# Performance work log

Measured on AMD Instinct MI355X. Metric: run time of the kernel, lower is better.

## Reference

```python
import jax, jax.numpy as jnp
import numpy as np
from jax import lax

D_MODEL = 2048
D_STATE = 16
D_CONV = 4
B_SZ = 2
T_LEN = 2048


def setup_inputs() -> dict:
    key = jax.random.key(0)
    ks = jax.random.split(key, 8)
    x = jax.random.normal(ks[0], (B_SZ, T_LEN, D_MODEL), dtype=jnp.float32)
    h = jnp.zeros((B_SZ, D_MODEL, D_STATE), dtype=jnp.float32)
    norm_w = jnp.ones((D_MODEL,), dtype=jnp.float32)
    in_proj_w = jax.random.normal(ks[1], (2 * D_MODEL, D_MODEL), dtype=jnp.float32) * (D_MODEL ** -0.5)
    conv_w = jax.random.normal(ks[2], (D_MODEL, 1, D_CONV), dtype=jnp.float32) * 0.5
    conv_b = jnp.zeros((D_MODEL,), dtype=jnp.float32)
    x_proj_w = jax.random.normal(ks[3], (D_MODEL + 2 * D_STATE, D_MODEL), dtype=jnp.float32) * (D_MODEL ** -0.5)
    A_log = jnp.broadcast_to(jnp.log(jnp.arange(1, D_STATE + 1, dtype=jnp.float32))[None, :], (D_MODEL, D_STATE)).copy()
    D = jnp.ones((D_MODEL,), dtype=jnp.float32)
    out_proj_w = jax.random.normal(ks[4], (D_MODEL, D_MODEL), dtype=jnp.float32) * (D_MODEL ** -0.5)
    return {"x": x, "h": h, "norm_w": norm_w, "in_proj_w": in_proj_w,
            "conv_w": conv_w, "conv_b": conv_b, "x_proj_w": x_proj_w,
            "A_log": A_log, "D": D, "out_proj_w": out_proj_w}


def _rmsnorm(x, w, eps=1e-6):
    ms = jnp.mean(jnp.square(x.astype(jnp.float32)), axis=-1, keepdims=True)
    return (x * lax.rsqrt(ms + eps).astype(x.dtype)) * w.astype(x.dtype)


def reference(x, h, norm_w, in_proj_w, conv_w, conv_b, x_proj_w, A_log, D, out_proj_w):
    B, T, d_model = x.shape
    d_state = A_log.shape[1]
    residual = x
    x_normed = _rmsnorm(x, norm_w)
    xz = x_normed @ in_proj_w.T                      # (B, T, 2*d_model)
    x_branch, z = jnp.split(xz, 2, axis=-1)
    # depthwise causal conv1d: torch pads both sides by d_conv-1 then slices [:T],
    # equivalent to left-pad-only causal conv.
    xc = x_branch.transpose(0, 2, 1)                 # (B, d_model, T)
    xc = lax.conv_general_dilated(
        xc, conv_w, window_strides=(1,), padding=[(D_CONV - 1, 0)],
        dimension_numbers=("NCH", "OIH", "NCH"), feature_group_count=d_model)
    xc = xc + conv_b[None, :, None]
    x_ssm = jax.nn.silu(xc.transpose(0, 2, 1))       # (B, T, d_model)

    # SSM core
    proj = x_ssm @ x_proj_w.T                        # (B, T, d_model + 2*d_state)
    delta_raw = proj[..., :d_model]
    B_in = proj[..., d_model:d_model + d_state]
    C_in = proj[..., d_model + d_state:]
    delta = jax.nn.softplus(delta_raw)               # (B, T, d_model)
    A = -jnp.exp(A_log.astype(jnp.float32))          # (d_model, d_state)

    def step(h_c, inp):
        d_t, b_t, c_t, x_t = inp                     # (B,dm) (B,ds) (B,ds) (B,dm)
        A_bar = jnp.exp(d_t[:, :, None] * A[None])   # (B, dm, ds)
        h_c = A_bar * h_c + (d_t * x_t)[:, :, None] * b_t[:, None, :]
        y_t = jnp.einsum("bdn,bn->bd", h_c, c_t) + D * x_t
        return h_c, y_t

    xs = (delta.transpose(1, 0, 2), B_in.transpose(1, 0, 2),
          C_in.transpose(1, 0, 2), x_ssm.transpose(1, 0, 2))
    h_new, ys = lax.scan(step, h.astype(x.dtype), xs)
    y = ys.transpose(1, 0, 2)                        # (B, T, d_model)

    y = y * jax.nn.silu(z)
    out = residual + y @ out_proj_w.T
    return out, lax.stop_gradient(h_new)
```

## Files before the change

### kernel.cpp

```cpp
#include <hip/hip_runtime.h>
#include <cstdint>
#include <cstddef>


typedef __bf16 bf16_t;
typedef __attribute__((ext_vector_type(8))) __bf16 bf16x8;
typedef __attribute__((ext_vector_type(4))) __bf16 bf16x4;
typedef __attribute__((ext_vector_type(4))) float f32x4;

#define D_MODEL 2048
#define D_STATE 16
#define B_SZ 2
#define T_LEN 2048
#define N_ROWS (B_SZ * T_LEN)
#define N_PAD  2176
#define N_CHUNK 32
#define L_CHUNK (T_LEN / N_CHUNK)
#define LOG2E 1.4426950408889634f

__device__ __forceinline__ void load_lds16(const void* g, void* l) {
    __builtin_amdgcn_global_load_lds(
        (const __attribute__((address_space(1))) void*)(uintptr_t)g,
        (__attribute__((address_space(3))) void*)(uintptr_t)l,
        16, 0, 0);
}

__global__ __launch_bounds__(256) void cast_w13(
    const float* __restrict__ w1, const float* __restrict__ w3,
    bf16_t* __restrict__ d1, bf16_t* __restrict__ d3)
{
    int i = blockIdx.x * 256 + threadIdx.x;
    const int n1 = 4096 * 2048 / 4;
    if (i < n1) {
        f32x4 v = ((const f32x4*)w1)[i];
        ((bf16x4*)d1)[i] = __builtin_convertvector(v, bf16x4);
    } else {
        int j = i - n1;
        f32x4 v = ((const f32x4*)w3)[j];
        ((bf16x4*)d3)[j] = __builtin_convertvector(v, bf16x4);
    }
}

__global__ __launch_bounds__(256) void cast_pad_w2(
    const float* __restrict__ s, bf16_t* __restrict__ d)
{
    int i = blockIdx.x * 256 + threadIdx.x;
    int row = i >> 11;
    int col = i & 2047;
    float v = (row < 2080) ? s[(size_t)row * 2048 + col] : 0.f;
    d[i] = (bf16_t)v;
}

__global__ __launch_bounds__(256) void rmsnorm_kernel(
    const float* __restrict__ x, const float* __restrict__ w,
    bf16_t* __restrict__ xn)
{
    int row = blockIdx.x;
    int tid = threadIdx.x;
    const float* xr = x + (size_t)row * D_MODEL;
    float ss = 0.f;
    for (int i = tid; i < D_MODEL; i += 256) { float v = xr[i]; ss = fmaf(v, v, ss); }
    #pragma unroll
    for (int o = 32; o > 0; o >>= 1) ss += __shfl_down(ss, o, 64);
    __shared__ float red[4];
    if ((tid & 63) == 0) red[tid >> 6] = ss;
    __syncthreads();
    float tot = red[0] + red[1] + red[2] + red[3];
    float scale = rsqrtf(tot * (1.f / D_MODEL) + 1e-6f);
    bf16_t* xo = xn + (size_t)row * D_MODEL;
    for (int i = tid; i < D_MODEL; i += 256) xo[i] = (bf16_t)(xr[i] * scale * w[i]);
}

template<int MODE>
__global__ __launch_bounds__(256) void gemm_bt(
    const bf16_t* __restrict__ A, const bf16_t* __restrict__ B, int K,
    float* __restrict__ out0, bf16_t* __restrict__ out1,
    const float* __restrict__ add)
{
    __shared__ __align__(16) bf16_t lA[128 * 32];
    __shared__ __align__(16) bf16_t lB[128 * 32];
    __shared__ __align__(16) float cs[32 * 132];
    const int tid = threadIdx.x;
    const int bm = blockIdx.x, bn = blockIdx.y;

    const int rA = tid >> 2;
    const int cA = (tid & 3) * 8;
    const bf16_t* aSrc = A + ((size_t)bm * 128 + rA) * K + cA;
    const bf16_t* bSrc = B + ((size_t)bn * 128 + rA) * K + cA;

    const int lane = tid & 63;
    const int wave = tid >> 6;
    const int wm = (wave & 1) * 64;
    const int wn = (wave >> 1) * 64;
    const int fr = lane & 15;
    const int quad = lane >> 4;
    const int aOff = (wm + fr) * 32 + quad * 8;
    const int bOff = (wn + fr) * 32 + quad * 8;

    f32x4 acc[4][4];
    #pragma unroll
    for (int i = 0; i < 4; ++i)
        #pragma unroll
        for (int j = 0; j < 4; ++j) acc[i][j] = {0.f, 0.f, 0.f, 0.f};

    const int kIters = K >> 5;
    for (int kt = 0; kt < kIters; ++kt) {
        load_lds16(aSrc,                  &lA[tid * 8]);
        load_lds16(aSrc + (size_t)64 * K, &lA[2048 + tid * 8]);
        load_lds16(bSrc,                  &lB[tid * 8]);
        load_lds16(bSrc + (size_t)64 * K, &lB[2048 + tid * 8]);
        aSrc += 32; bSrc += 32;
        __syncthreads();

        bf16x8 af[4], bv[4];
        #pragma unroll
        for (int i = 0; i < 4; ++i) af[i] = *(const bf16x8*)(&lA[aOff + i * 512]);
        #pragma unroll
        for (int j = 0; j < 4; ++j) bv[j] = *(const bf16x8*)(&lB[bOff + j * 512]);
        #pragma unroll
        for (int i = 0; i < 4; ++i)
            #pragma unroll
            for (int j = 0; j < 4; ++j)
                acc[i][j] = __builtin_amdgcn_mfma_f32_16x16x32_bf16(
                    af[i], bv[j], acc[i][j], 0, 0, 0);
        __syncthreads();
    }

    const int lrow0 = (wave & 1) * 16 + quad * 4;
    const int lcol0 = wn + fr;
    for (int i = 0; i < 4; ++i) {
        __syncthreads();
        #pragma unroll
        for (int j = 0; j < 4; ++j)
            #pragma unroll
            for (int rr = 0; rr < 4; ++rr)
                cs[(lrow0 + rr) * 132 + lcol0 + j * 16] = acc[i][j][rr];
        __syncthreads();
        #pragma unroll
        for (int k = 0; k < 4; ++k) {
            int f4  = tid + k * 256;
            int row = f4 >> 5;
            int c4  = (f4 & 31) * 4;
            f32x4 v = *(const f32x4*)&cs[row * 132 + c4];
            int gr = bm * 128 + i * 16 + ((row < 16) ? row : (48 + row));
            int gc = bn * 128 + c4;
            if (MODE == 0) {
                if (bn < 16) {
                    *(f32x4*)&out0[(size_t)gr * 2048 + gc] = v;
                } else {
                    bf16x4 o;
                    #pragma unroll
                    for (int e = 0; e < 4; ++e) {
                        float s = v[e];
                        o[e] = (bf16_t)(s / (1.f + __expf(-s)));
                    }
                    *(bf16x4*)&out1[(size_t)gr * 2048 + (gc - 2048)] = o;
                }
            } else if (MODE == 1) {
                if (bn < 16) {
                    #pragma unroll
                    for (int e = 0; e < 4; ++e) {
                        float s = v[e];
                        v[e] = fmaxf(s, 0.f) + __logf(1.f + __expf(-fabsf(s)));
                    }
                }
                *(f32x4*)&out0[(size_t)gr * N_PAD + gc] = v;
            } else {
                f32x4 a4 = *(const f32x4*)&add[(size_t)gr * 2048 + gc];
                v = v + a4;
                *(f32x4*)&out0[(size_t)gr * 2048 + gc] = v;
            }
        }
    }
}

__global__ __launch_bounds__(256) void conv_silu_kernel(
    const float* __restrict__ xb, const float* __restrict__ cw,
    const float* __restrict__ cb, bf16_t* __restrict__ xs_b)
{
    int id = blockIdx.x * 256 + threadIdx.x;
    int d  = id & 2047;
    int tb = (id >> 11) & 255;
    int b  = id >> 19;
    float w0 = cw[d * 4 + 0], w1 = cw[d * 4 + 1], w2 = cw[d * 4 + 2], w3 = cw[d * 4 + 3];
    float bias = cb[d];
    int t0 = tb * 8;
    size_t base = (size_t)b * T_LEN;
    float v[11];
    #pragma unroll
    for (int i = 0; i < 11; ++i) {
        int t = t0 - 3 + i;
        v[i] = (t >= 0) ? xb[(base + t) * 2048 + d] : 0.f;
    }
    #pragma unroll
    for (int j = 0; j < 8; ++j) {
        float s = bias + w0 * v[j] + w1 * v[j + 1] + w2 * v[j + 2] + w3 * v[j + 3];
        float sl = s / (1.f + __expf(-s));
        xs_b[(base + t0 + j) * D_MODEL + d] = (bf16_t)sl;
    }
}

#define PF 4

__global__ __launch_bounds__(256) void scan_phase1(
    const float* __restrict__ proj, const bf16_t* __restrict__ xs,
    const float* __restrict__ A_log,
    float* __restrict__ Aprod, float* __restrict__ hfin)
{
    int wi   = blockIdx.x * 4 + (threadIdx.x >> 6);
    int lane = threadIdx.x & 63;
    int nq   = lane & 3;
    int dsub = lane >> 2;
    int c  = wi & 31;
    int dg = (wi >> 5) & 127;
    int b  = wi >> 12;
    int dd = dg * 16 + dsub;

    float A2[4], h[4], Ap[4];
    #pragma unroll
    for (int j = 0; j < 4; ++j) {
        A2[j] = -__expf(A_log[dd * D_STATE + nq * 4 + j]) * LOG2E;
        h[j] = 0.f; Ap[j] = 1.f;
    }
    const int t0 = c * L_CHUNK;
    const int tmax = t0 + L_CHUNK - 1;

    float p_da[PF], p_xv[PF];
    f32x4 p_B[PF];
    #pragma unroll
    for (int u = 0; u < PF; ++u) {
        size_t row = (size_t)b * T_LEN + t0 + u;
        const float* pr = proj + row * N_PAD;
        p_da[u] = pr[dd];
        p_xv[u] = (float)xs[row * D_MODEL + dd];
        p_B[u]  = *(const f32x4*)(pr + D_MODEL + nq * 4);
    }

    for (int it = 0; it < L_CHUNK; it += PF) {
        #pragma unroll
        for (int u = 0; u < PF; ++u) {
            int t = t0 + it + u;
            float da = p_da[u], xv = p_xv[u];
            f32x4 Bv = p_B[u];
            int tn = t + PF; tn = (tn > tmax) ? tmax : tn;
            {
                size_t row = (size_t)b * T_LEN + tn;
                const float* pr = proj + row * N_PAD;
                p_da[u] = pr[dd];
                p_xv[u] = (float)xs[row * D_MODEL + dd];
                p_B[u]  = *(const f32x4*)(pr + D_MODEL + nq * 4);
            }
            float dx = da * xv;
            #pragma unroll
            for (int j = 0; j < 4; ++j) {
                float a = exp2f(da * A2[j]);
                Ap[j] *= a;
                h[j] = fmaf(a, h[j], dx * Bv[j]);
            }
        }
    }
    size_t o = ((size_t)c * 4096 + b * 2048 + dd) * D_STATE + nq * 4;
    *(f32x4*)(Aprod + o) = f32x4{Ap[0], Ap[1], Ap[2], Ap[3]};
    *(f32x4*)(hfin  + o) = f32x4{h[0], h[1], h[2], h[3]};
}

__global__ __launch_bounds__(256) void scan_phase2(
    const float* __restrict__ h_in, const float* __restrict__ Aprod,
    float* __restrict__ hfin, float* __restrict__ h_out)
{
    int g = blockIdx.x * 256 + threadIdx.x;
    float h = h_in[g];
    for (int c = 0; c < N_CHUNK; ++c) {
        size_t o = (size_t)c * 65536 + g;
        float a   = Aprod[o];
        float loc = hfin[o];
        hfin[o] = h;
        h = fmaf(a, h, loc);
    }
    h_out[g] = h;
}

__global__ __launch_bounds__(256) void scan_phase3(
    const float* __restrict__ proj, const bf16_t* __restrict__ xs,
    const bf16_t* __restrict__ zg, const float* __restrict__ A_log,
    const float* __restrict__ Dv, const float* __restrict__ hinit,
    bf16_t* __restrict__ yg)
{
    int wi   = blockIdx.x * 4 + (threadIdx.x >> 6);
    int lane = threadIdx.x & 63;
    int nq   = lane & 3;
    int dsub = lane >> 2;
    int c  = wi & 31;
    int dg = (wi >> 5) & 127;
    int b  = wi >> 12;
    int dd = dg * 16 + dsub;

    float A2[4], h[4];
    size_t o = ((size_t)c * 4096 + b * 2048 + dd) * D_STATE + nq * 4;
    #pragma unroll
    for (int j = 0; j < 4; ++j) {
        A2[j] = -__expf(A_log[dd * D_STATE + nq * 4 + j]) * LOG2E;
        h[j]  = hinit[o + j];
    }
    float Dd = Dv[dd];
    const int t0 = c * L_CHUNK;
    const int tmax = t0 + L_CHUNK - 1;

    float p_da[PF], p_xv[PF], p_sz[PF];
    f32x4 p_B[PF], p_C[PF];
    #pragma unroll
    for (int u = 0; u < PF; ++u) {
        size_t row = (size_t)b * T_LEN + t0 + u;
        const float* pr = proj + row * N_PAD;
        p_da[u] = pr[dd];
        p_xv[u] = (float)xs[row * D_MODEL + dd];
        p_sz[u] = (float)zg[row * 2048 + dd];
        p_B[u]  = *(const f32x4*)(pr + D_MODEL + nq * 4);
        p_C[u]  = *(const f32x4*)(pr + D_MODEL + D_STATE + nq * 4);
    }

    for (int it = 0; it < L_CHUNK; it += PF) {
        #pragma unroll
        for (int u = 0; u < PF; ++u) {
            int t = t0 + it + u;
            float da = p_da[u], xv = p_xv[u], sz = p_sz[u];
            f32x4 Bv = p_B[u], Cv = p_C[u];
            int tn = t + PF; tn = (tn > tmax) ? tmax : tn;
            {
                size_t row = (size_t)b * T_LEN + tn;
                const float* pr = proj + row * N_PAD;
                p_da[u] = pr[dd];
                p_xv[u] = (float)xs[row * D_MODEL + dd];
                p_sz[u] = (float)zg[row * 2048 + dd];
                p_B[u]  = *(const f32x4*)(pr + D_MODEL + nq * 4);
                p_C[u]  = *(const f32x4*)(pr + D_MODEL + D_STATE + nq * 4);
            }
            float dx = da * xv;
            float yp = 0.f;
            #pragma unroll
            for (int j = 0; j < 4; ++j) {
                float a = exp2f(da * A2[j]);
                h[j] = fmaf(a, h[j], dx * Bv[j]);
                yp = fmaf(h[j], Cv[j], yp);
            }
            yp += __shfl_xor(yp, 1, 64);
            yp += __shfl_xor(yp, 2, 64);
            if (nq == 0) {
                float y = fmaf(Dd, xv, yp);
                yg[((size_t)b * T_LEN + t) * D_MODEL + dd] = (bf16_t)(y * sz);
            }
        }
    }
}

extern "C" void kernel_launch(void* const* d_in, const int* in_sizes, int n_in,
                              void* d_out, int out_size, void* d_ws, size_t ws_size,
                              hipStream_t stream)
{
    const float* x    = (const float*)d_in[0];
    const float* h0   = (const float*)d_in[1];
    const float* nw   = (const float*)d_in[2];
    const float* w_in = (const float*)d_in[3];
    const float* cw   = (const float*)d_in[4];
    const float* cb   = (const float*)d_in[5];
    const float* w_x  = (const float*)d_in[6];
    const float* alog = (const float*)d_in[7];
    const float* dv   = (const float*)d_in[8];
    const float* w_out= (const float*)d_in[9];
    float* out  = (float*)d_out;
    float* hout = out + (size_t)N_ROWS * D_MODEL;

    char* ws = (char*)d_ws;
    size_t off = 0;
    auto alloc = [&](size_t bytes) -> void* {
        void* p = ws + off;
        off += (bytes + 255) & ~(size_t)255;
        return p;
    };
    bf16_t* W1  = (bf16_t*)alloc((size_t)4096 * 2048 * 2);
    bf16_t* W2  = (bf16_t*)alloc((size_t)N_PAD * 2048 * 2);
    bf16_t* W3  = (bf16_t*)alloc((size_t)2048 * 2048 * 2);
    bf16_t* XN  = (bf16_t*)alloc((size_t)N_ROWS * 2048 * 2);
    float*  XB  = (float*) alloc((size_t)N_ROWS * 2048 * 4);
    bf16_t* ZG  = (bf16_t*)alloc((size_t)N_ROWS * 2048 * 2);
    float*  PROJ= (float*) alloc((size_t)N_ROWS * N_PAD * 4);
    float* APROD= (float*) alloc((size_t)N_CHUNK * 4096 * D_STATE * 4);
    float* HFIN = (float*) alloc((size_t)N_CHUNK * 4096 * D_STATE * 4);
    bf16_t* XSb = W1;
    bf16_t* YG  = XN;

    cast_w13<<<(4096 * 2048 / 4 + 2048 * 2048 / 4) / 256, 256, 0, stream>>>(w_in, w_out, W1, W3);
    cast_pad_w2<<<(N_PAD * 2048) / 256, 256, 0, stream>>>(w_x, W2);

    rmsnorm_kernel<<<N_ROWS, 256, 0, stream>>>(x, nw, XN);
    gemm_bt<0><<<dim3(32, 32), 256, 0, stream>>>(XN, W1, 2048, XB, ZG, nullptr);
    conv_silu_kernel<<<(B_SZ * (T_LEN / 8) * D_MODEL) / 256, 256, 0, stream>>>(XB, cw, cb, XSb);
    gemm_bt<1><<<dim3(32, N_PAD / 128), 256, 0, stream>>>(XSb, W2, 2048, PROJ, nullptr, nullptr);
    scan_phase1<<<2048, 256, 0, stream>>>(PROJ, XSb, alog, APROD, HFIN);
    scan_phase2<<<256, 256, 0, stream>>>(h0, APROD, HFIN, hout);
    scan_phase3<<<2048, 256, 0, stream>>>(PROJ, XSb, ZG, alog, dv, HFIN, YG);
    gemm_bt<2><<<dim3(32, 16), 256, 0, stream>>>(YG, W3, 2048, out, nullptr, x);

    (void)in_sizes; (void)n_in; (void)out_size; (void)ws_size;
}
```

Measured before the change: 515.8 us.

## Rewrite bf16 GEMM with 256x256 tiles and 4-stage LDS pipeline; vectorize rmsnorm

The MFMA GEMM moves to 512-thread blocks that compute 256x256 output tiles. It uses a 4-deep ring of global_load_lds stages with explicit vmcnt waits, so there is one barrier per k-step instead of two. It adds a swizzled LDS layout to avoid bank conflicts, raises wave priority around the MFMA burst, and uses a wider epilogue staging buffer. N_PAD grows to 2304 so the x_proj GEMM fits the larger tiles, which costs some extra padded work. The 128 KB LDS footprint allows only one block per CU, and the out_proj grid shrinks to 128 blocks, which leaves many CUs idle. The rmsnorm kernel now keeps each row in float4 registers and writes bf16x4 vectors.

```diff
diff --git a/kernel.cpp b/kernel.cpp
--- a/kernel.cpp
+++ b/kernel.cpp
@@ -13,7 +13,7 @@
 #define B_SZ 2
 #define T_LEN 2048
 #define N_ROWS (B_SZ * T_LEN)
-#define N_PAD  2176
+#define N_PAD  2304
 #define N_CHUNK 32
 #define L_CHUNK (T_LEN / N_CHUNK)
 #define LOG2E 1.4426950408889634f
@@ -24,6 +24,9 @@
         (__attribute__((address_space(3))) void*)(uintptr_t)l,
         16, 0, 0);
 }
+
+#define VMW(n) asm volatile("s_waitcnt vmcnt(" #n ")" ::: "memory")
+#define BAR()  do { __builtin_amdgcn_s_barrier(); __builtin_amdgcn_sched_barrier(0); } while (0)
 
 __global__ __launch_bounds__(256) void cast_w13(
     const float* __restrict__ w1, const float* __restrict__ w3,
@@ -57,9 +60,12 @@
 {
     int row = blockIdx.x;
     int tid = threadIdx.x;
-    const float* xr = x + (size_t)row * D_MODEL;
+    const f32x4* xr = (const f32x4*)(x + (size_t)row * D_MODEL);
+    f32x4 v0 = xr[tid];
+    f32x4 v1 = xr[tid + 256];
     float ss = 0.f;
-    for (int i = tid; i < D_MODEL; i += 256) { float v = xr[i]; ss = fmaf(v, v, ss); }
+    #pragma unroll
+    for (int e = 0; e < 4; ++e) { ss = fmaf(v0[e], v0[e], ss); ss = fmaf(v1[e], v1[e], ss); }
     #pragma unroll
     for (int o = 32; o > 0; o >>= 1) ss += __shfl_down(ss, o, 64);
     __shared__ float red[4];
@@ -67,110 +73,139 @@
     __syncthreads();
     float tot = red[0] + red[1] + red[2] + red[3];
     float scale = rsqrtf(tot * (1.f / D_MODEL) + 1e-6f);
-    bf16_t* xo = xn + (size_t)row * D_MODEL;
-    for (int i = tid; i < D_MODEL; i += 256) xo[i] = (bf16_t)(xr[i] * scale * w[i]);
+    const f32x4* w4 = (const f32x4*)w;
+    f32x4 m0 = v0 * w4[tid] * scale;
+    f32x4 m1 = v1 * w4[tid + 256] * scale;
+    bf16x4* xo = (bf16x4*)(xn + (size_t)row * D_MODEL);
+    xo[tid]       = __builtin_convertvector(m0, bf16x4);
+    xo[tid + 256] = __builtin_convertvector(m1, bf16x4);
 }
 
 template<int MODE>
-__global__ __launch_bounds__(256) void gemm_bt(
-    const bf16_t* __restrict__ A, const bf16_t* __restrict__ B, int K,
+__global__ __launch_bounds__(512, 2) void gemm_bt(
+    const bf16_t* __restrict__ A, const bf16_t* __restrict__ Bw, int K,
     float* __restrict__ out0, bf16_t* __restrict__ out1,
     const float* __restrict__ add)
 {
-    __shared__ __align__(16) bf16_t lA[128 * 32];
-    __shared__ __align__(16) bf16_t lB[128 * 32];
-    __shared__ __align__(16) float cs[32 * 132];
-    const int tid = threadIdx.x;
-    const int bm = blockIdx.x, bn = blockIdx.y;
-
-    const int rA = tid >> 2;
-    const int cA = (tid & 3) * 8;
-    const bf16_t* aSrc = A + ((size_t)bm * 128 + rA) * K + cA;
-    const bf16_t* bSrc = B + ((size_t)bn * 128 + rA) * K + cA;
-
+    __shared__ __align__(16) char smem[131072];
+    char* const ldsA = smem;
+    char* const ldsB = smem + 65536;
+
+    const int tid  = threadIdx.x;
+    const int bm   = blockIdx.x, bn = blockIdx.y;
     const int lane = tid & 63;
     const int wave = tid >> 6;
-    const int wm = (wave & 1) * 64;
-    const int wn = (wave >> 1) * 64;
-    const int fr = lane & 15;
+    const int wm   = wave >> 2;
+    const int wn   = wave & 3;
+    const int fr   = lane & 15;
     const int quad = lane >> 4;
-    const int aOff = (wm + fr) * 32 + quad * 8;
-    const int bOff = (wn + fr) * 32 + quad * 8;
-
-    f32x4 acc[4][4];
-    #pragma unroll
-    for (int i = 0; i < 4; ++i)
+
+    const int rS   = tid >> 2;
+    const int cS   = tid & 3;
+    const int gcol = ((cS - ((rS >> 1) & 3)) & 3) * 8;
+    const bf16_t* sA0 = A  + (size_t)(bm * 256 + rS) * K + gcol;
+    const bf16_t* sA1 = sA0 + (size_t)128 * K;
+    const bf16_t* sB0 = Bw + (size_t)(bn * 256 + rS) * K + gcol;
+    const bf16_t* sB1 = sB0 + (size_t)128 * K;
+
+    const int swz  = ((quad + ((fr >> 1) & 3)) & 3) * 8;
+    const int aOff = (wm * 128 + fr) * 32 + swz;
+    const int bOff = (wn * 64  + fr) * 32 + swz;
+
+    f32x4 acc[8][4];
+    #pragma unroll
+    for (int i = 0; i < 8; ++i)
         #pragma unroll
         for (int j = 0; j < 4; ++j) acc[i][j] = {0.f, 0.f, 0.f, 0.f};
 
-    const int kIters = K >> 5;
-    for (int kt = 0; kt < kIters; ++kt) {
-        load_lds16(aSrc,                  &lA[tid * 8]);
-        load_lds16(aSrc + (size_t)64 * K, &lA[2048 + tid * 8]);
-        load_lds16(bSrc,                  &lB[tid * 8]);
-        load_lds16(bSrc + (size_t)64 * K, &lB[2048 + tid * 8]);
-        aSrc += 32; bSrc += 32;
-        __syncthreads();
-
-        bf16x8 af[4], bv[4];
-        #pragma unroll
-        for (int i = 0; i < 4; ++i) af[i] = *(const bf16x8*)(&lA[aOff + i * 512]);
-        #pragma unroll
-        for (int j = 0; j < 4; ++j) bv[j] = *(const bf16x8*)(&lB[bOff + j * 512]);
-        #pragma unroll
-        for (int i = 0; i < 4; ++i)
+#define STAGE(b) do { \
+        load_lds16(sA0, ldsA + (b) * 16384 + tid * 16);        \
+        load_lds16(sA1, ldsA + (b) * 16384 + tid * 16 + 8192); \
+        load_lds16(sB0, ldsB + (b) * 16384 + tid * 16);        \
+        load_lds16(sB1, ldsB + (b) * 16384 + tid * 16 + 8192); \
+        sA0 += 32; sA1 += 32; sB0 += 32; sB1 += 32; } while (0)
+
+    auto compute = [&](int cb) {
+        const bf16_t* pA = (const bf16_t*)(ldsA + cb * 16384);
+        const bf16_t* pB = (const bf16_t*)(ldsB + cb * 16384);
+        bf16x8 bfr[4];
+        #pragma unroll
+        for (int j = 0; j < 4; ++j)
+            bfr[j] = *(const bf16x8*)(pB + bOff + j * 512);
+        __builtin_amdgcn_s_setprio(1);
+        #pragma unroll
+        for (int i = 0; i < 8; ++i) {
+            bf16x8 a = *(const bf16x8*)(pA + aOff + i * 512);
             #pragma unroll
             for (int j = 0; j < 4; ++j)
                 acc[i][j] = __builtin_amdgcn_mfma_f32_16x16x32_bf16(
-                    af[i], bv[j], acc[i][j], 0, 0, 0);
+                    a, bfr[j], acc[i][j], 0, 0, 0);
+        }
+        __builtin_amdgcn_s_setprio(0);
+    };
+
+    const int nt = K >> 5;
+    STAGE(0); STAGE(1); STAGE(2);
+    for (int t = 0; t < nt - 3; ++t) {
+        VMW(8); BAR();
+        STAGE((t + 3) & 3);
+        compute(t & 3);
+    }
+    VMW(8); BAR(); compute((nt - 3) & 3);
+    VMW(4); BAR(); compute((nt - 2) & 3);
+    VMW(0); BAR(); compute((nt - 1) & 3);
+#undef STAGE
+
+    float* const cs = (float*)smem;
+    __syncthreads();
+    for (int s = 0; s < 4; ++s) {
+        if (wm == (s >> 1)) {
+            const int i0 = (s & 1) * 4;
+            #pragma unroll
+            for (int ii = 0; ii < 4; ++ii)
+                #pragma unroll
+                for (int j = 0; j < 4; ++j)
+                    #pragma unroll
+                    for (int rr = 0; rr < 4; ++rr)
+                        cs[(ii * 16 + quad * 4 + rr) * 268 + wn * 64 + j * 16 + fr]
+                            = acc[i0 + ii][j][rr];
+        }
         __syncthreads();
-    }
-
-    const int lrow0 = (wave & 1) * 16 + quad * 4;
-    const int lcol0 = wn + fr;
-    for (int i = 0; i < 4; ++i) {
-        __syncthreads();
-        #pragma unroll
-        for (int j = 0; j < 4; ++j)
-            #pragma unroll
-            for (int rr = 0; rr < 4; ++rr)
-                cs[(lrow0 + rr) * 132 + lcol0 + j * 16] = acc[i][j][rr];
-        __syncthreads();
-        #pragma unroll
-        for (int k = 0; k < 4; ++k) {
-            int f4  = tid + k * 256;
-            int row = f4 >> 5;
-            int c4  = (f4 & 31) * 4;
-            f32x4 v = *(const f32x4*)&cs[row * 132 + c4];
-            int gr = bm * 128 + i * 16 + ((row < 16) ? row : (48 + row));
-            int gc = bn * 128 + c4;
+        #pragma unroll
+        for (int k = 0; k < 8; ++k) {
+            const int idx = tid + k * 512;
+            const int row = idx >> 6;
+            const int c4  = (idx & 63) << 2;
+            f32x4 v = *(const f32x4*)(cs + row * 268 + c4);
+            const int gr = bm * 256 + s * 64 + row;
+            const int gc = bn * 256 + c4;
             if (MODE == 0) {
-                if (bn < 16) {
+                if (bn < 8) {
                     *(f32x4*)&out0[(size_t)gr * 2048 + gc] = v;
                 } else {
                     bf16x4 o;
                     #pragma unroll
                     for (int e = 0; e < 4; ++e) {
-                        float s = v[e];
-                        o[e] = (bf16_t)(s / (1.f + __expf(-s)));
+                        float sv = v[e];
+                        o[e] = (bf16_t)(sv / (1.f + __expf(-sv)));
                     }
                     *(bf16x4*)&out1[(size_t)gr * 2048 + (gc - 2048)] = o;
                 }
             } else if (MODE == 1) {
-                if (bn < 16) {
+                if (bn < 8) {
                     #pragma unroll
                     for (int e = 0; e < 4; ++e) {
-                        float s = v[e];
-                        v[e] = fmaxf(s, 0.f) + __logf(1.f + __expf(-fabsf(s)));
+                        float sv = v[e];
+                        v[e] = fmaxf(sv, 0.f) + __logf(1.f + __expf(-fabsf(sv)));
                     }
                 }
                 *(f32x4*)&out0[(size_t)gr * N_PAD + gc] = v;
             } else {
                 f32x4 a4 = *(const f32x4*)&add[(size_t)gr * 2048 + gc];
-                v = v + a4;
-                *(f32x4*)&out0[(size_t)gr * 2048 + gc] = v;
+                *(f32x4*)&out0[(size_t)gr * 2048 + gc] = v + a4;
             }
         }
+        __syncthreads();
     }
 }
 
@@ -393,13 +428,13 @@
     cast_pad_w2<<<(N_PAD * 2048) / 256, 256, 0, stream>>>(w_x, W2);
 
     rmsnorm_kernel<<<N_ROWS, 256, 0, stream>>>(x, nw, XN);
-    gemm_bt<0><<<dim3(32, 32), 256, 0, stream>>>(XN, W1, 2048, XB, ZG, nullptr);
+    gemm_bt<0><<<dim3(16, 16), 512, 0, stream>>>(XN, W1, 2048, XB, ZG, nullptr);
     conv_silu_kernel<<<(B_SZ * (T_LEN / 8) * D_MODEL) / 256, 256, 0, stream>>>(XB, cw, cb, XSb);
-    gemm_bt<1><<<dim3(32, N_PAD / 128), 256, 0, stream>>>(XSb, W2, 2048, PROJ, nullptr, nullptr);
+    gemm_bt<1><<<dim3(16, N_PAD / 256), 512, 0, stream>>>(XSb, W2, 2048, PROJ, nullptr, nullptr);
     scan_phase1<<<2048, 256, 0, stream>>>(PROJ, XSb, alog, APROD, HFIN);
     scan_phase2<<<256, 256, 0, stream>>>(h0, APROD, HFIN, hout);
     scan_phase3<<<2048, 256, 0, stream>>>(PROJ, XSb, ZG, alog, dv, HFIN, YG);
-    gemm_bt<2><<<dim3(32, 16), 256, 0, stream>>>(YG, W3, 2048, out, nullptr, x);
+    gemm_bt<2><<<dim3(16, 8), 512, 0, stream>>>(YG, W3, 2048, out, nullptr, x);
 
     (void)in_sizes; (void)n_in; (void)out_size; (void)ws_size;
 }
```

New measurement: 531.0 us. 3.0% more time.
